# Kernel tuning notes

Hardware: AMD Instinct MI355X
Metric: run time of the kernel (lower is better)

The kernel has to match this reference:

```python
import jax, jax.numpy as jnp
import numpy as np

EMBED = 1024
HEADS = 16
HEAD_DIM = EMBED // HEADS
NEG = -1e20


def setup_inputs() -> dict:
    key = jax.random.key(0)
    ks = jax.random.split(key, 12)
    N, L = 2, 2048
    lim_h = 1.0 / np.sqrt(HEAD_DIM)
    lim_e = 1.0 / np.sqrt(EMBED)
    u = lambda k, shape, lim: jax.random.uniform(k, shape, jnp.float32, -lim, lim)
    return {
        "query": jax.random.normal(ks[0], (N, L, EMBED), jnp.float32),
        "key": jax.random.normal(ks[1], (N, L, EMBED), jnp.float32),
        "value": jax.random.normal(ks[2], (N, L, EMBED), jnp.float32),
        "mask": jax.random.randint(ks[3], (N, 1, L, L), 0, 2, jnp.int32),
        "Wq": u(ks[4], (HEAD_DIM, HEAD_DIM), lim_h),
        "bq": u(ks[5], (HEAD_DIM,), lim_h),
        "Wk": u(ks[6], (HEAD_DIM, HEAD_DIM), lim_h),
        "bk": u(ks[7], (HEAD_DIM,), lim_h),
        "Wv": u(ks[8], (HEAD_DIM, HEAD_DIM), lim_h),
        "bv": u(ks[9], (HEAD_DIM,), lim_h),
        "Wo": u(ks[10], (EMBED, EMBED), lim_e),
        "bo": u(ks[11], (EMBED,), lim_e),
    }


def reference(query, key, value, mask, Wq, bq, Wk, bk, Wv, bv, Wo, bo):
    N, Lq, _ = query.shape
    Lk = key.shape[1]
    # split heads: [N, L, H, D]
    q = query.reshape(N, Lq, HEADS, HEAD_DIM)
    k = key.reshape(N, Lk, HEADS, HEAD_DIM)
    v = value.reshape(N, Lk, HEADS, HEAD_DIM)
    # shared per-head linear projections (torch Linear: x @ W.T + b)
    q = jnp.einsum('nlhd,ed->nlhe', q, Wq) + bq
    k = jnp.einsum('nlhd,ed->nlhe', k, Wk) + bk
    v = jnp.einsum('nlhd,ed->nlhe', v, Wv) + bv
    # scores [N, H, Q, K]
    energy = jnp.einsum('nqhd,nkhd->nhqk', q, k)
    # NOTE: original masks BEFORE scaling, and scales by sqrt(embed_size)
    energy = jnp.where(mask == 0, NEG, energy)
    energy = energy / jnp.sqrt(jnp.float32(EMBED))
    attn = jax.nn.softmax(energy, axis=-1)
    out = jnp.einsum('nhqk,nkhd->nqhd', attn, v)
    out = out.reshape(N, Lq, EMBED)
    return out @ Wo.T + bo
```

## Files before the change

### kernel.cpp

```cpp
#include <hip/hip_runtime.h>

#define NBATCH 2
#define SEQ 2048
#define EMBED 1024
#define HEADS 16
#define HDIM 64

typedef short s16x8 __attribute__((ext_vector_type(8)));
typedef float f32x4 __attribute__((ext_vector_type(4)));
typedef unsigned short u16;

__device__ __forceinline__ u16 f2bf(float f) {
    union { float f; unsigned u; } v; v.f = f;
    unsigned r = v.u + 0x7FFFu + ((v.u >> 16) & 1u);
    return (u16)(r >> 16);
}
__device__ __forceinline__ s16x8 f8bf(const float* p) {
    const float4 a = *(const float4*)p;
    const float4 b = *(const float4*)(p + 4);
    s16x8 r;
    r[0] = (short)f2bf(a.x); r[1] = (short)f2bf(a.y);
    r[2] = (short)f2bf(a.z); r[3] = (short)f2bf(a.w);
    r[4] = (short)f2bf(b.x); r[5] = (short)f2bf(b.y);
    r[6] = (short)f2bf(b.z); r[7] = (short)f2bf(b.w);
    return r;
}

__global__ __launch_bounds__(256) void proj_kernel(
    const float* __restrict__ x, const float* __restrict__ W,
    const float* __restrict__ bias, u16* __restrict__ out, int transpose)
{
    const int wv = threadIdx.x >> 6;
    const int lane = threadIdx.x & 63;
    const int lr = lane & 15, lg = lane >> 4;
    const int nh = blockIdx.y, n = nh >> 4, h = nh & 15;
    const int lbase = blockIdx.x * 64 + wv * 16;

    const float* xrow = x + ((size_t)(n * SEQ + lbase + lr)) * EMBED + h * HDIM;
    const s16x8 a0 = f8bf(xrow + lg * 8);
    const s16x8 a1 = f8bf(xrow + 32 + lg * 8);

#pragma unroll
    for (int eb = 0; eb < 4; ++eb) {
        const float* wrow = W + (eb * 16 + lr) * HDIM;
        const s16x8 b0 = f8bf(wrow + lg * 8);
        const s16x8 b1 = f8bf(wrow + 32 + lg * 8);
        f32x4 c = {0.f, 0.f, 0.f, 0.f};
        c = __builtin_amdgcn_mfma_f32_16x16x32_bf16(a0, b0, c, 0, 0, 0);
        c = __builtin_amdgcn_mfma_f32_16x16x32_bf16(a1, b1, c, 0, 0, 0);
        const int col = eb * 16 + lr;
        const float bv = bias[col];
        if (!transpose) {
#pragma unroll
            for (int r = 0; r < 4; ++r) {
                const int row = lbase + lg * 4 + r;
                out[((size_t)nh * SEQ + row) * HDIM + col] = f2bf(c[r] + bv);
            }
        } else {
#pragma unroll
            for (int r = 0; r < 4; ++r) {
                const int row = lbase + lg * 4 + r;
                out[((size_t)nh * HDIM + col) * SEQ + row] = f2bf(c[r] + bv);
            }
        }
    }
}

__global__ __launch_bounds__(256) void attn_kernel(
    const float* __restrict__ xq, const float* __restrict__ Wq,
    const float* __restrict__ bq,
    const u16* __restrict__ Kp, const u16* __restrict__ Vt,
    const int* __restrict__ mask, float* __restrict__ Xo)
{
    __shared__ __align__(16) u16 qlds[4][16 * 64];
    __shared__ __align__(16) u16 plds[4][16 * 32];
    const int wv = threadIdx.x >> 6;
    const int lane = threadIdx.x & 63;
    const int lr = lane & 15, lg = lane >> 4;
    const int nh = blockIdx.y, n = nh >> 4, h = nh & 15;
    const int qbase = blockIdx.x * 64 + wv * 16;

    {
        const float* xrow = xq + ((size_t)(n * SEQ + qbase + lr)) * EMBED + h * HDIM;
        const s16x8 a0 = f8bf(xrow + lg * 8);
        const s16x8 a1 = f8bf(xrow + 32 + lg * 8);
#pragma unroll
        for (int eb = 0; eb < 4; ++eb) {
            const float* wrow = Wq + (eb * 16 + lr) * HDIM;
            const s16x8 b0 = f8bf(wrow + lg * 8);
            const s16x8 b1 = f8bf(wrow + 32 + lg * 8);
            f32x4 c = {0.f, 0.f, 0.f, 0.f};
            c = __builtin_amdgcn_mfma_f32_16x16x32_bf16(a0, b0, c, 0, 0, 0);
            c = __builtin_amdgcn_mfma_f32_16x16x32_bf16(a1, b1, c, 0, 0, 0);
            const int col = eb * 16 + lr;
            const float bv = bq[col];
#pragma unroll
            for (int r = 0; r < 4; ++r)
                qlds[wv][(lg * 4 + r) * 64 + col] = f2bf(c[r] + bv);
        }
    }
    __syncthreads();
    const s16x8 aq0 = *(const s16x8*)(&qlds[wv][lr * 64 + lg * 8]);
    const s16x8 aq1 = *(const s16x8*)(&qlds[wv][lr * 64 + 32 + lg * 8]);

    const int* mbase = mask + (size_t)n * SEQ * SEQ;
    const u16* vbase = Vt + (size_t)nh * HDIM * SEQ;

    float m_[4], ls[4];
    f32x4 o_[4];
#pragma unroll
    for (int r = 0; r < 4; ++r) { m_[r] = -1e30f; ls[r] = 0.f; }
#pragma unroll
    for (int db = 0; db < 4; ++db) o_[db] = (f32x4){0.f, 0.f, 0.f, 0.f};

    const float inv32 = 1.0f / 32.0f;
    const float NEGS  = -3.125e18f;
    u16* pb = plds[wv];

    for (int kb = 0; kb < SEQ; kb += 32) {
        const u16* krow0 = Kp + ((size_t)nh * SEQ + kb + lr) * HDIM;
        const u16* krow1 = krow0 + 16 * HDIM;
        f32x4 s0 = {0.f, 0.f, 0.f, 0.f}, s1 = {0.f, 0.f, 0.f, 0.f};
        s0 = __builtin_amdgcn_mfma_f32_16x16x32_bf16(aq0, *(const s16x8*)(krow0 + lg * 8), s0, 0, 0, 0);
        s0 = __builtin_amdgcn_mfma_f32_16x16x32_bf16(aq1, *(const s16x8*)(krow0 + 32 + lg * 8), s0, 0, 0, 0);
        s1 = __builtin_amdgcn_mfma_f32_16x16x32_bf16(aq0, *(const s16x8*)(krow1 + lg * 8), s1, 0, 0, 0);
        s1 = __builtin_amdgcn_mfma_f32_16x16x32_bf16(aq1, *(const s16x8*)(krow1 + 32 + lg * 8), s1, 0, 0, 0);

        float tm[4];
#pragma unroll
        for (int r = 0; r < 4; ++r) {
            const int qr = qbase + lg * 4 + r;
            const int* mp = mbase + (size_t)qr * SEQ + kb;
            s0[r] = mp[lr]      ? s0[r] * inv32 : NEGS;
            s1[r] = mp[16 + lr] ? s1[r] * inv32 : NEGS;
            tm[r] = fmaxf(s0[r], s1[r]);
        }
#pragma unroll
        for (int off = 1; off < 16; off <<= 1)
#pragma unroll
            for (int r = 0; r < 4; ++r) tm[r] = fmaxf(tm[r], __shfl_xor(tm[r], off));

        float sc[4], rs[4];
        f32x4 p0, p1;
#pragma unroll
        for (int r = 0; r < 4; ++r) {
            const float mn = fmaxf(m_[r], tm[r]);
            sc[r] = __expf(m_[r] - mn);
            m_[r] = mn;
            p0[r] = __expf(s0[r] - mn);
            p1[r] = __expf(s1[r] - mn);
            rs[r] = p0[r] + p1[r];
        }
#pragma unroll
        for (int off = 1; off < 16; off <<= 1)
#pragma unroll
            for (int r = 0; r < 4; ++r) rs[r] += __shfl_xor(rs[r], off);
#pragma unroll
        for (int r = 0; r < 4; ++r) ls[r] = ls[r] * sc[r] + rs[r];
#pragma unroll
        for (int db = 0; db < 4; ++db)
#pragma unroll
            for (int r = 0; r < 4; ++r) o_[db][r] *= sc[r];

        __syncthreads();
#pragma unroll
        for (int r = 0; r < 4; ++r) {
            pb[(lg * 4 + r) * 32 + lr]      = f2bf(p0[r]);
            pb[(lg * 4 + r) * 32 + 16 + lr] = f2bf(p1[r]);
        }
        __syncthreads();
        const s16x8 pa = *(const s16x8*)(pb + lr * 32 + lg * 8);

#pragma unroll
        for (int db = 0; db < 4; ++db) {
            const s16x8 vb = *(const s16x8*)(vbase + (size_t)(db * 16 + lr) * SEQ + kb + lg * 8);
            o_[db] = __builtin_amdgcn_mfma_f32_16x16x32_bf16(pa, vb, o_[db], 0, 0, 0);
        }
    }

#pragma unroll
    for (int r = 0; r < 4; ++r) {
        const float inv = 1.0f / ls[r];
        const int qr = qbase + lg * 4 + r;
        float* orow = Xo + ((size_t)n * SEQ + qr) * EMBED + h * HDIM;
#pragma unroll
        for (int db = 0; db < 4; ++db)
            orow[db * 16 + lr] = o_[db][r] * inv;
    }
}

__global__ __launch_bounds__(256) void outproj_valu(
    const float* __restrict__ X, const float* __restrict__ Wo,
    const float* __restrict__ bo, float* __restrict__ out)
{
    __shared__ float xs[64][33];
    __shared__ float wt[64][33];
    const int rbase = blockIdx.y * 64, cbase = blockIdx.x * 64;
    const int t = threadIdx.x;
    const int rg = t >> 4, cg = t & 15;

    float acc[4][4];
#pragma unroll
    for (int i = 0; i < 4; ++i)
#pragma unroll
        for (int j = 0; j < 4; ++j) acc[i][j] = 0.f;

    for (int e0 = 0; e0 < EMBED; e0 += 32) {
        __syncthreads();
        for (int idx = t; idx < 64 * 32; idx += 256) {
            const int rl = idx >> 5, el = idx & 31;
            xs[rl][el] = X[(size_t)(rbase + rl) * EMBED + e0 + el];
            wt[rl][el] = Wo[(size_t)(cbase + rl) * EMBED + e0 + el];
        }
        __syncthreads();
#pragma unroll 8
        for (int e = 0; e < 32; ++e) {
            float xv[4], wv[4];
#pragma unroll
            for (int i = 0; i < 4; ++i) xv[i] = xs[rg * 4 + i][e];
#pragma unroll
            for (int j = 0; j < 4; ++j) wv[j] = wt[cg * 4 + j][e];
#pragma unroll
            for (int i = 0; i < 4; ++i)
#pragma unroll
                for (int j = 0; j < 4; ++j) acc[i][j] += xv[i] * wv[j];
        }
    }
#pragma unroll
    for (int i = 0; i < 4; ++i) {
        const int r = rbase + rg * 4 + i;
#pragma unroll
        for (int j = 0; j < 4; ++j) {
            const int c = cbase + cg * 4 + j;
            out[(size_t)r * EMBED + c] = acc[i][j] + bo[c];
        }
    }
}

extern "C" void kernel_launch(void* const* d_in, const int* in_sizes, int n_in,
                              void* d_out, int out_size, void* d_ws, size_t ws_size,
                              hipStream_t stream)
{
    const float* q    = (const float*)d_in[0];
    const float* k    = (const float*)d_in[1];
    const float* v    = (const float*)d_in[2];
    const int*  mask  = (const int*)d_in[3];
    const float* Wq   = (const float*)d_in[4];
    const float* bq   = (const float*)d_in[5];
    const float* Wk   = (const float*)d_in[6];
    const float* bk   = (const float*)d_in[7];
    const float* Wv   = (const float*)d_in[8];
    const float* bv   = (const float*)d_in[9];
    const float* Wo   = (const float*)d_in[10];
    const float* bo   = (const float*)d_in[11];

    u16* ws = (u16*)d_ws;
    const size_t per = (size_t)NBATCH * HEADS * SEQ * HDIM;
    u16*   Kp  = ws;
    u16*   Vt  = ws + per;
    float* Xof = (float*)(ws + 2 * per);

    const dim3 pgrid(SEQ / 64, NBATCH * HEADS);
    proj_kernel<<<pgrid, 256, 0, stream>>>(k, Wk, bk, Kp, 0);
    proj_kernel<<<pgrid, 256, 0, stream>>>(v, Wv, bv, Vt, 1);
    attn_kernel<<<dim3(SEQ / 64, NBATCH * HEADS), 256, 0, stream>>>(q, Wq, bq, Kp, Vt, mask, Xof);
    outproj_valu<<<dim3(EMBED / 64, NBATCH * SEQ / 64), 256, 0, stream>>>(Xof, Wo, bo, (float*)d_out);
}
```

Before: 590.3 us.

## Bit-pack mask, switch to fp16, widen attention tiles, MFMA output projection

Packs the int32 mask into 64-bit bitmasks with a ballot kernel, so attention reads one word per row per 64 keys instead of 64 ints. All bf16 paths become fp16 MFMA. Attention now processes 64 keys per step, replaces block-wide syncthreads with per-wave lgkmcnt waits, and XOR-swizzles the shared-memory layouts. The scalar fp32 output projection is replaced by an fp16 MFMA GEMM fed by a new Wo conversion kernel and an fp16 attention output. The trade-offs are reduced fp16 precision, two extra kernel launches, and reliance on wave-private LDS with no barrier.

```diff
diff --git a/kernel.cpp b/kernel.cpp
--- a/kernel.cpp
+++ b/kernel.cpp
@@ -6,29 +6,46 @@
 #define HEADS 16
 #define HDIM 64
 
-typedef short s16x8 __attribute__((ext_vector_type(8)));
+typedef _Float16 h16x8 __attribute__((ext_vector_type(8)));
+typedef _Float16 h16x4 __attribute__((ext_vector_type(4)));
 typedef float f32x4 __attribute__((ext_vector_type(4)));
-typedef unsigned short u16;
-
-__device__ __forceinline__ u16 f2bf(float f) {
-    union { float f; unsigned u; } v; v.f = f;
-    unsigned r = v.u + 0x7FFFu + ((v.u >> 16) & 1u);
-    return (u16)(r >> 16);
-}
-__device__ __forceinline__ s16x8 f8bf(const float* p) {
+typedef unsigned long long u64;
+
+__device__ __forceinline__ h16x8 f8h(const float* p) {
     const float4 a = *(const float4*)p;
     const float4 b = *(const float4*)(p + 4);
-    s16x8 r;
-    r[0] = (short)f2bf(a.x); r[1] = (short)f2bf(a.y);
-    r[2] = (short)f2bf(a.z); r[3] = (short)f2bf(a.w);
-    r[4] = (short)f2bf(b.x); r[5] = (short)f2bf(b.y);
-    r[6] = (short)f2bf(b.z); r[7] = (short)f2bf(b.w);
+    h16x8 r;
+    r[0] = (_Float16)a.x; r[1] = (_Float16)a.y;
+    r[2] = (_Float16)a.z; r[3] = (_Float16)a.w;
+    r[4] = (_Float16)b.x; r[5] = (_Float16)b.y;
+    r[6] = (_Float16)b.z; r[7] = (_Float16)b.w;
     return r;
+}
+
+__global__ __launch_bounds__(256) void maskpack(const int* __restrict__ m,
+                                                u64* __restrict__ mb)
+{
+    const size_t i = (size_t)blockIdx.x * 256 + threadIdx.x;
+    const u64 b = __ballot(m[i] != 0);
+    if ((threadIdx.x & 63) == 0) mb[i >> 6] = b;
+}
+
+__global__ __launch_bounds__(256) void cvt16(const float* __restrict__ in,
+                                             _Float16* __restrict__ out, int n)
+{
+    const int i = (blockIdx.x * 256 + threadIdx.x) * 4;
+    if (i < n) {
+        const float4 v = *(const float4*)(in + i);
+        h16x4 o;
+        o[0] = (_Float16)v.x; o[1] = (_Float16)v.y;
+        o[2] = (_Float16)v.z; o[3] = (_Float16)v.w;
+        *(h16x4*)(out + i) = o;
+    }
 }
 
 __global__ __launch_bounds__(256) void proj_kernel(
     const float* __restrict__ x, const float* __restrict__ W,
-    const float* __restrict__ bias, u16* __restrict__ out, int transpose)
+    const float* __restrict__ bias, _Float16* __restrict__ out, int transpose)
 {
     const int wv = threadIdx.x >> 6;
     const int lane = threadIdx.x & 63;
@@ -37,30 +54,30 @@
     const int lbase = blockIdx.x * 64 + wv * 16;
 
     const float* xrow = x + ((size_t)(n * SEQ + lbase + lr)) * EMBED + h * HDIM;
-    const s16x8 a0 = f8bf(xrow + lg * 8);
-    const s16x8 a1 = f8bf(xrow + 32 + lg * 8);
+    const h16x8 a0 = f8h(xrow + lg * 8);
+    const h16x8 a1 = f8h(xrow + 32 + lg * 8);
 
 #pragma unroll
     for (int eb = 0; eb < 4; ++eb) {
         const float* wrow = W + (eb * 16 + lr) * HDIM;
-        const s16x8 b0 = f8bf(wrow + lg * 8);
-        const s16x8 b1 = f8bf(wrow + 32 + lg * 8);
+        const h16x8 b0 = f8h(wrow + lg * 8);
+        const h16x8 b1 = f8h(wrow + 32 + lg * 8);
         f32x4 c = {0.f, 0.f, 0.f, 0.f};
-        c = __builtin_amdgcn_mfma_f32_16x16x32_bf16(a0, b0, c, 0, 0, 0);
-        c = __builtin_amdgcn_mfma_f32_16x16x32_bf16(a1, b1, c, 0, 0, 0);
+        c = __builtin_amdgcn_mfma_f32_16x16x32_f16(a0, b0, c, 0, 0, 0);
+        c = __builtin_amdgcn_mfma_f32_16x16x32_f16(a1, b1, c, 0, 0, 0);
         const int col = eb * 16 + lr;
         const float bv = bias[col];
         if (!transpose) {
 #pragma unroll
             for (int r = 0; r < 4; ++r) {
                 const int row = lbase + lg * 4 + r;
-                out[((size_t)nh * SEQ + row) * HDIM + col] = f2bf(c[r] + bv);
+                out[((size_t)nh * SEQ + row) * HDIM + col] = (_Float16)(c[r] + bv);
             }
         } else {
 #pragma unroll
             for (int r = 0; r < 4; ++r) {
                 const int row = lbase + lg * 4 + r;
-                out[((size_t)nh * HDIM + col) * SEQ + row] = f2bf(c[r] + bv);
+                out[((size_t)nh * HDIM + col) * SEQ + row] = (_Float16)(c[r] + bv);
             }
         }
     }
@@ -69,42 +86,49 @@
 __global__ __launch_bounds__(256) void attn_kernel(
     const float* __restrict__ xq, const float* __restrict__ Wq,
     const float* __restrict__ bq,
-    const u16* __restrict__ Kp, const u16* __restrict__ Vt,
-    const int* __restrict__ mask, float* __restrict__ Xo)
-{
-    __shared__ __align__(16) u16 qlds[4][16 * 64];
-    __shared__ __align__(16) u16 plds[4][16 * 32];
+    const _Float16* __restrict__ Kp, const _Float16* __restrict__ Vt,
+    const u64* __restrict__ mbits, _Float16* __restrict__ Xo)
+{
+    __shared__ __align__(16) _Float16 qlds[4][16 * 64];
+    __shared__ __align__(16) _Float16 plds[4][16 * 64];
     const int wv = threadIdx.x >> 6;
     const int lane = threadIdx.x & 63;
     const int lr = lane & 15, lg = lane >> 4;
     const int nh = blockIdx.y, n = nh >> 4, h = nh & 15;
     const int qbase = blockIdx.x * 64 + wv * 16;
 
+    _Float16* qb_ = qlds[wv];
+    _Float16* pb_ = plds[wv];
+
     {
         const float* xrow = xq + ((size_t)(n * SEQ + qbase + lr)) * EMBED + h * HDIM;
-        const s16x8 a0 = f8bf(xrow + lg * 8);
-        const s16x8 a1 = f8bf(xrow + 32 + lg * 8);
+        const h16x8 a0 = f8h(xrow + lg * 8);
+        const h16x8 a1 = f8h(xrow + 32 + lg * 8);
 #pragma unroll
         for (int eb = 0; eb < 4; ++eb) {
             const float* wrow = Wq + (eb * 16 + lr) * HDIM;
-            const s16x8 b0 = f8bf(wrow + lg * 8);
-            const s16x8 b1 = f8bf(wrow + 32 + lg * 8);
+            const h16x8 b0 = f8h(wrow + lg * 8);
+            const h16x8 b1 = f8h(wrow + 32 + lg * 8);
             f32x4 c = {0.f, 0.f, 0.f, 0.f};
-            c = __builtin_amdgcn_mfma_f32_16x16x32_bf16(a0, b0, c, 0, 0, 0);
-            c = __builtin_amdgcn_mfma_f32_16x16x32_bf16(a1, b1, c, 0, 0, 0);
+            c = __builtin_amdgcn_mfma_f32_16x16x32_f16(a0, b0, c, 0, 0, 0);
+            c = __builtin_amdgcn_mfma_f32_16x16x32_f16(a1, b1, c, 0, 0, 0);
             const int col = eb * 16 + lr;
             const float bv = bq[col];
 #pragma unroll
-            for (int r = 0; r < 4; ++r)
-                qlds[wv][(lg * 4 + r) * 64 + col] = f2bf(c[r] + bv);
-        }
-    }
-    __syncthreads();
-    const s16x8 aq0 = *(const s16x8*)(&qlds[wv][lr * 64 + lg * 8]);
-    const s16x8 aq1 = *(const s16x8*)(&qlds[wv][lr * 64 + 32 + lg * 8]);
-
-    const int* mbase = mask + (size_t)n * SEQ * SEQ;
-    const u16* vbase = Vt + (size_t)nh * HDIM * SEQ;
+            for (int r = 0; r < 4; ++r) {
+                const int row = lg * 4 + r;
+                qb_[(row * 64 + col) ^ ((row & 7) << 3)] = (_Float16)(c[r] + bv);
+            }
+        }
+    }
+    asm volatile("s_waitcnt lgkmcnt(0)" ::: "memory");
+    __builtin_amdgcn_sched_barrier(0);
+    const h16x8 aq0 = *(const h16x8*)(qb_ + ((lr * 64 + lg * 8) ^ ((lr & 7) << 3)));
+    const h16x8 aq1 = *(const h16x8*)(qb_ + ((lr * 64 + 32 + lg * 8) ^ ((lr & 7) << 3)));
+
+    const u64* mrow = mbits + (size_t)n * SEQ * (SEQ / 64);
+    const _Float16* kbase = Kp + (size_t)nh * SEQ * HDIM;
+    const _Float16* vbase = Vt + (size_t)nh * HDIM * SEQ;
 
     float m_[4], ls[4];
     f32x4 o_[4];
@@ -115,25 +139,31 @@
 
     const float inv32 = 1.0f / 32.0f;
     const float NEGS  = -3.125e18f;
-    u16* pb = plds[wv];
-
-    for (int kb = 0; kb < SEQ; kb += 32) {
-        const u16* krow0 = Kp + ((size_t)nh * SEQ + kb + lr) * HDIM;
-        const u16* krow1 = krow0 + 16 * HDIM;
-        f32x4 s0 = {0.f, 0.f, 0.f, 0.f}, s1 = {0.f, 0.f, 0.f, 0.f};
-        s0 = __builtin_amdgcn_mfma_f32_16x16x32_bf16(aq0, *(const s16x8*)(krow0 + lg * 8), s0, 0, 0, 0);
-        s0 = __builtin_amdgcn_mfma_f32_16x16x32_bf16(aq1, *(const s16x8*)(krow0 + 32 + lg * 8), s0, 0, 0, 0);
-        s1 = __builtin_amdgcn_mfma_f32_16x16x32_bf16(aq0, *(const s16x8*)(krow1 + lg * 8), s1, 0, 0, 0);
-        s1 = __builtin_amdgcn_mfma_f32_16x16x32_bf16(aq1, *(const s16x8*)(krow1 + 32 + lg * 8), s1, 0, 0, 0);
+
+    for (int kb = 0; kb < SEQ; kb += 64) {
+        f32x4 s[4];
+#pragma unroll
+        for (int sg = 0; sg < 4; ++sg) {
+            const _Float16* kr = kbase + (size_t)(kb + sg * 16 + lr) * HDIM;
+            f32x4 c = {0.f, 0.f, 0.f, 0.f};
+            c = __builtin_amdgcn_mfma_f32_16x16x32_f16(aq0, *(const h16x8*)(kr + lg * 8), c, 0, 0, 0);
+            c = __builtin_amdgcn_mfma_f32_16x16x32_f16(aq1, *(const h16x8*)(kr + 32 + lg * 8), c, 0, 0, 0);
+            s[sg] = c;
+        }
 
         float tm[4];
 #pragma unroll
         for (int r = 0; r < 4; ++r) {
             const int qr = qbase + lg * 4 + r;
-            const int* mp = mbase + (size_t)qr * SEQ + kb;
-            s0[r] = mp[lr]      ? s0[r] * inv32 : NEGS;
-            s1[r] = mp[16 + lr] ? s1[r] * inv32 : NEGS;
-            tm[r] = fmaxf(s0[r], s1[r]);
+            const u64 mw = mrow[(size_t)qr * (SEQ / 64) + (kb >> 6)];
+            float t = -3.0e38f;
+#pragma unroll
+            for (int sg = 0; sg < 4; ++sg) {
+                const bool on = (mw >> (sg * 16 + lr)) & 1ull;
+                s[sg][r] = on ? s[sg][r] * inv32 : NEGS;
+                t = fmaxf(t, s[sg][r]);
+            }
+            tm[r] = t;
         }
 #pragma unroll
         for (int off = 1; off < 16; off <<= 1)
@@ -141,16 +171,22 @@
             for (int r = 0; r < 4; ++r) tm[r] = fmaxf(tm[r], __shfl_xor(tm[r], off));
 
         float sc[4], rs[4];
-        f32x4 p0, p1;
 #pragma unroll
         for (int r = 0; r < 4; ++r) {
             const float mn = fmaxf(m_[r], tm[r]);
             sc[r] = __expf(m_[r] - mn);
             m_[r] = mn;
-            p0[r] = __expf(s0[r] - mn);
-            p1[r] = __expf(s1[r] - mn);
-            rs[r] = p0[r] + p1[r];
-        }
+            rs[r] = 0.f;
+        }
+#pragma unroll
+        for (int sg = 0; sg < 4; ++sg)
+#pragma unroll
+            for (int r = 0; r < 4; ++r) {
+                const float p = __expf(s[sg][r] - m_[r]);
+                rs[r] += p;
+                const int row = lg * 4 + r;
+                pb_[(row * 64 + sg * 16 + lr) ^ ((row & 7) << 3)] = (_Float16)p;
+            }
 #pragma unroll
         for (int off = 1; off < 16; off <<= 1)
 #pragma unroll
@@ -162,19 +198,16 @@
 #pragma unroll
             for (int r = 0; r < 4; ++r) o_[db][r] *= sc[r];
 
-        __syncthreads();
-#pragma unroll
-        for (int r = 0; r < 4; ++r) {
-            pb[(lg * 4 + r) * 32 + lr]      = f2bf(p0[r]);
-            pb[(lg * 4 + r) * 32 + 16 + lr] = f2bf(p1[r]);
-        }
-        __syncthreads();
-        const s16x8 pa = *(const s16x8*)(pb + lr * 32 + lg * 8);
+        asm volatile("s_waitcnt lgkmcnt(0)" ::: "memory");
+        __builtin_amdgcn_sched_barrier(0);
+        const h16x8 pa0 = *(const h16x8*)(pb_ + ((lr * 64 + lg * 8) ^ ((lr & 7) << 3)));
+        const h16x8 pa1 = *(const h16x8*)(pb_ + ((lr * 64 + 32 + lg * 8) ^ ((lr & 7) << 3)));
 
 #pragma unroll
         for (int db = 0; db < 4; ++db) {
-            const s16x8 vb = *(const s16x8*)(vbase + (size_t)(db * 16 + lr) * SEQ + kb + lg * 8);
-            o_[db] = __builtin_amdgcn_mfma_f32_16x16x32_bf16(pa, vb, o_[db], 0, 0, 0);
+            const _Float16* vr = vbase + (size_t)(db * 16 + lr) * SEQ + kb;
+            o_[db] = __builtin_amdgcn_mfma_f32_16x16x32_f16(pa0, *(const h16x8*)(vr + lg * 8), o_[db], 0, 0, 0);
+            o_[db] = __builtin_amdgcn_mfma_f32_16x16x32_f16(pa1, *(const h16x8*)(vr + 32 + lg * 8), o_[db], 0, 0, 0);
         }
     }
 
@@ -182,57 +215,44 @@
     for (int r = 0; r < 4; ++r) {
         const float inv = 1.0f / ls[r];
         const int qr = qbase + lg * 4 + r;
-        float* orow = Xo + ((size_t)n * SEQ + qr) * EMBED + h * HDIM;
+        _Float16* orow = Xo + ((size_t)n * SEQ + qr) * EMBED + h * HDIM;
 #pragma unroll
         for (int db = 0; db < 4; ++db)
-            orow[db * 16 + lr] = o_[db][r] * inv;
-    }
-}
-
-__global__ __launch_bounds__(256) void outproj_valu(
-    const float* __restrict__ X, const float* __restrict__ Wo,
+            orow[db * 16 + lr] = (_Float16)(o_[db][r] * inv);
+    }
+}
+
+__global__ __launch_bounds__(256) void outproj_mfma(
+    const _Float16* __restrict__ X, const _Float16* __restrict__ Wo16,
     const float* __restrict__ bo, float* __restrict__ out)
 {
-    __shared__ float xs[64][33];
-    __shared__ float wt[64][33];
-    const int rbase = blockIdx.y * 64, cbase = blockIdx.x * 64;
-    const int t = threadIdx.x;
-    const int rg = t >> 4, cg = t & 15;
-
-    float acc[4][4];
-#pragma unroll
-    for (int i = 0; i < 4; ++i)
-#pragma unroll
-        for (int j = 0; j < 4; ++j) acc[i][j] = 0.f;
-
-    for (int e0 = 0; e0 < EMBED; e0 += 32) {
-        __syncthreads();
-        for (int idx = t; idx < 64 * 32; idx += 256) {
-            const int rl = idx >> 5, el = idx & 31;
-            xs[rl][el] = X[(size_t)(rbase + rl) * EMBED + e0 + el];
-            wt[rl][el] = Wo[(size_t)(cbase + rl) * EMBED + e0 + el];
-        }
-        __syncthreads();
-#pragma unroll 8
-        for (int e = 0; e < 32; ++e) {
-            float xv[4], wv[4];
-#pragma unroll
-            for (int i = 0; i < 4; ++i) xv[i] = xs[rg * 4 + i][e];
-#pragma unroll
-            for (int j = 0; j < 4; ++j) wv[j] = wt[cg * 4 + j][e];
-#pragma unroll
-            for (int i = 0; i < 4; ++i)
-#pragma unroll
-                for (int j = 0; j < 4; ++j) acc[i][j] += xv[i] * wv[j];
-        }
-    }
-#pragma unroll
-    for (int i = 0; i < 4; ++i) {
-        const int r = rbase + rg * 4 + i;
-#pragma unroll
-        for (int j = 0; j < 4; ++j) {
-            const int c = cbase + cg * 4 + j;
-            out[(size_t)r * EMBED + c] = acc[i][j] + bo[c];
+    const int wv = threadIdx.x >> 6;
+    const int lane = threadIdx.x & 63;
+    const int lr = lane & 15, lg = lane >> 4;
+    const int rbase = blockIdx.y * 64 + wv * 16;
+    const int cbase = blockIdx.x * 64;
+
+    f32x4 acc[4];
+#pragma unroll
+    for (int cb = 0; cb < 4; ++cb) acc[cb] = (f32x4){0.f, 0.f, 0.f, 0.f};
+
+    const _Float16* xrow = X + (size_t)(rbase + lr) * EMBED;
+    for (int k0 = 0; k0 < EMBED; k0 += 32) {
+        const h16x8 a = *(const h16x8*)(xrow + k0 + lg * 8);
+#pragma unroll
+        for (int cb = 0; cb < 4; ++cb) {
+            const h16x8 b = *(const h16x8*)(Wo16 + (size_t)(cbase + cb * 16 + lr) * EMBED + k0 + lg * 8);
+            acc[cb] = __builtin_amdgcn_mfma_f32_16x16x32_f16(a, b, acc[cb], 0, 0, 0);
+        }
+    }
+#pragma unroll
+    for (int cb = 0; cb < 4; ++cb) {
+        const int col = cbase + cb * 16 + lr;
+        const float bv = bo[col];
+#pragma unroll
+        for (int r = 0; r < 4; ++r) {
+            const int row = rbase + lg * 4 + r;
+            out[(size_t)row * EMBED + col] = acc[cb][r] + bv;
         }
     }
 }
@@ -254,15 +274,19 @@
     const float* Wo   = (const float*)d_in[10];
     const float* bo   = (const float*)d_in[11];
 
-    u16* ws = (u16*)d_ws;
     const size_t per = (size_t)NBATCH * HEADS * SEQ * HDIM;
-    u16*   Kp  = ws;
-    u16*   Vt  = ws + per;
-    float* Xof = (float*)(ws + 2 * per);
-
+    const size_t nmask = (size_t)NBATCH * SEQ * SEQ;
+    u64*      mbits = (u64*)d_ws;
+    _Float16* Kp    = (_Float16*)(mbits + nmask / 64);
+    _Float16* Vt    = Kp + per;
+    _Float16* Xh    = Vt + per;
+    _Float16* Wo16  = Xh + per;
+
+    maskpack<<<(int)(nmask / 256), 256, 0, stream>>>(mask, mbits);
+    cvt16<<<EMBED * EMBED / 1024, 256, 0, stream>>>(Wo, Wo16, EMBED * EMBED);
     const dim3 pgrid(SEQ / 64, NBATCH * HEADS);
     proj_kernel<<<pgrid, 256, 0, stream>>>(k, Wk, bk, Kp, 0);
     proj_kernel<<<pgrid, 256, 0, stream>>>(v, Wv, bv, Vt, 1);
-    attn_kernel<<<dim3(SEQ / 64, NBATCH * HEADS), 256, 0, stream>>>(q, Wq, bq, Kp, Vt, mask, Xof);
-    outproj_valu<<<dim3(EMBED / 64, NBATCH * SEQ / 64), 256, 0, stream>>>(Xof, Wo, bo, (float*)d_out);
-}
+    attn_kernel<<<dim3(SEQ / 64, NBATCH * HEADS), 256, 0, stream>>>(q, Wq, bq, Kp, Vt, mbits, Xh);
+    outproj_mfma<<<dim3(EMBED / 64, NBATCH * SEQ / 64), 256, 0, stream>>>(Xh, Wo16, bo, (float*)d_out);
+}
```

Result: faster. 478.0 us (-19.0%).
